# Kernel optimization log

Hardware: AMD Instinct MI355X
Metric: run time of the kernel (lower is better)

Reference implementation:

```python
import jax, jax.numpy as jnp
import numpy as np

NEG_SLOPE = 0.2


def gat_conv(x, edge_index, W, att_src, att_dst, bias, concat):
    # PyG GATConv with add_self_loops=True, negative_slope=0.2
    N = x.shape[0]
    H, C = att_src.shape
    h = (x @ W).reshape(N, H, C)                      # [N, H, C]
    loops = jnp.arange(N, dtype=edge_index.dtype)
    src = jnp.concatenate([edge_index[0], loops])     # [E+N]
    dst = jnp.concatenate([edge_index[1], loops])
    a_src = jnp.einsum('nhc,hc->nh', h, att_src)      # [N, H]
    a_dst = jnp.einsum('nhc,hc->nh', h, att_dst)
    e = jax.nn.leaky_relu(a_src[src] + a_dst[dst], NEG_SLOPE)  # [E+N, H]
    # segment softmax over destination neighborhoods
    e_max = jax.ops.segment_max(e, dst, num_segments=N)        # [N, H]
    e_exp = jnp.exp(e - e_max[dst])
    denom = jax.ops.segment_sum(e_exp, dst, num_segments=N)    # [N, H]
    alpha = e_exp / denom[dst]                                  # [E+N, H]
    msg = h[src] * alpha[:, :, None]                            # [E+N, H, C]
    out = jax.ops.segment_sum(msg, dst, num_segments=N)        # [N, H, C]
    if concat:
        out = out.reshape(N, H * C)
    else:
        out = out.mean(axis=1)
    return out + bias


def setup_inputs() -> dict:
    key = jax.random.key(0)
    ks = jax.random.split(key, 12)
    N, E = 100000, 1600000
    IN, HID, HEADS = 8, 32, 4
    x = jax.random.normal(ks[0], (N, IN), dtype=jnp.float32)
    edge_index = jax.random.randint(ks[1], (2, E), 0, N, dtype=jnp.int32)
    s = 0.1
    W1 = jax.random.normal(ks[2], (IN, HEADS * HID), dtype=jnp.float32) * s
    att_src1 = jax.random.normal(ks[3], (HEADS, HID), dtype=jnp.float32) * s
    att_dst1 = jax.random.normal(ks[4], (HEADS, HID), dtype=jnp.float32) * s
    bias1 = jnp.zeros((HEADS * HID,), dtype=jnp.float32)
    W2 = jax.random.normal(ks[5], (HEADS * HID, HEADS * HID), dtype=jnp.float32) * s
    att_src2 = jax.random.normal(ks[6], (HEADS, HID), dtype=jnp.float32) * s
    att_dst2 = jax.random.normal(ks[7], (HEADS, HID), dtype=jnp.float32) * s
    bias2 = jnp.zeros((HID,), dtype=jnp.float32)
    W_lin = jax.random.normal(ks[8], (HID, 1), dtype=jnp.float32) * s
    b_lin = jnp.zeros((1,), dtype=jnp.float32)
    return {"x": x, "edge_index": edge_index,
            "W1": W1, "att_src1": att_src1, "att_dst1": att_dst1, "bias1": bias1,
            "W2": W2, "att_src2": att_src2, "att_dst2": att_dst2, "bias2": bias2,
            "W_lin": W_lin, "b_lin": b_lin}


def reference(x, edge_index, W1, att_src1, att_dst1, bias1,
              W2, att_src2, att_dst2, bias2, W_lin, b_lin):
    h = gat_conv(x, edge_index, W1, att_src1, att_dst1, bias1, concat=True)
    h = jax.nn.relu(h)
    # dropout p=0.2 is a no-op in eval mode
    h = gat_conv(h, edge_index, W2, att_src2, att_dst2, bias2, concat=False)
    h = jax.nn.relu(h)
    out = h @ W_lin + b_lin
    return out.reshape(-1)
```

## Files before the change

kernel.cpp:

```cpp
#include <hip/hip_runtime.h>

#define NEG_SLOPE 0.2f
#define K1 1024
#define S1B 512

typedef __attribute__((ext_vector_type(8))) short bf16x8;
typedef __attribute__((ext_vector_type(4))) float f32x4;

__device__ __forceinline__ unsigned short f2b(float f) {
    unsigned int u = __float_as_uint(f);
    u += 0x7FFFu + ((u >> 16) & 1u);
    return (unsigned short)(u >> 16);
}
__device__ __forceinline__ float blo(unsigned int u) { return __uint_as_float(u << 16); }
__device__ __forceinline__ float bhi(unsigned int u) { return __uint_as_float(u & 0xFFFF0000u); }

__global__ __launch_bounds__(256) void k_hist(
    const int* __restrict__ ei, int E, int EN,
    int* __restrict__ counts_t,
    const float* __restrict__ x, const float* __restrict__ W1,
    const float* __restrict__ as1, const float* __restrict__ ad1,
    float* __restrict__ asrc, float* __restrict__ adst,
    const float* __restrict__ W2, unsigned short* __restrict__ W2p,
    int N, int AB)
{
    int b = blockIdx.x;
    int t = threadIdx.x;
    if (b < S1B) {
        __shared__ int h[K1];
        for (int k = t; k < K1; k += 256) h[k] = 0;
        __syncthreads();
        int chunk = (EN + S1B - 1) / S1B;
        int lo = b * chunk, hi = min(lo + chunk, EN);
        for (int e = lo + t; e < hi; e += 256) {
            int dst = (e < E) ? ei[E + e] : (e - E);
            atomicAdd(&h[dst >> 7], 1);
        }
        __syncthreads();
        for (int k = t; k < K1; k += 256)
            counts_t[(size_t)k * S1B + b] = h[k];
        return;
    }
    if (b < S1B + AB) {
        __shared__ float s_wa[32], s_wd[32];
        if (t < 32) {
            int k = t >> 2, hh = t & 3;
            float sa = 0.f, sd = 0.f;
            for (int cc = 0; cc < 32; cc++) {
                float w = W1[k * 128 + hh * 32 + cc];
                sa = fmaf(w, as1[hh * 32 + cc], sa);
                sd = fmaf(w, ad1[hh * 32 + cc], sd);
            }
            s_wa[t] = sa;
            s_wd[t] = sd;
        }
        __syncthreads();
        int g = (b - S1B) * 256 + t;
        int n = g >> 2;
        if (n >= N) return;
        int hh = g & 3;
        const float* xr = x + (size_t)n * 8;
        float sa = 0.f, sd = 0.f;
        #pragma unroll
        for (int k = 0; k < 8; k++) {
            float xv = xr[k];
            sa = fmaf(xv, s_wa[k * 4 + hh], sa);
            sd = fmaf(xv, s_wd[k * 4 + hh], sd);
        }
        asrc[n * 4 + hh] = sa;
        adst[n * 4 + hh] = sd;
        return;
    }
    int w = t >> 6, lane = t & 63;
    int quad = lane >> 4, lanelo = lane & 15;
    int tile_n = b - S1B - AB;
    size_t base = (((size_t)tile_n * 4 + w) * 64 + lane) * 8;
    #pragma unroll
    for (int j = 0; j < 8; j++) {
        int k = w * 32 + quad * 8 + j;
        int n = tile_n * 16 + lanelo;
        W2p[base + j] = f2b(W2[k * 128 + n]);
    }
}

__global__ __launch_bounds__(S1B) void k_cscan(
    int* __restrict__ counts_t, int* __restrict__ T)
{
    __shared__ int s[S1B];
    int k = blockIdx.x, t = threadIdx.x;
    int v = counts_t[(size_t)k * S1B + t];
    s[t] = v;
    __syncthreads();
    for (int off = 1; off < S1B; off <<= 1) {
        int u = (t >= off) ? s[t - off] : 0;
        __syncthreads();
        s[t] += u;
        __syncthreads();
    }
    counts_t[(size_t)k * S1B + t] = s[t] - v;
    if (t == S1B - 1) T[k] = s[t];
}

__device__ __forceinline__ void tofs_scan(const int* __restrict__ T,
                                          int* sT, int* ps, int t)
{
    int base = t * 4;
    int s0 = T[base], s1 = T[base + 1], s2 = T[base + 2], s3 = T[base + 3];
    int tot = s0 + s1 + s2 + s3;
    ps[t] = tot;
    __syncthreads();
    for (int off = 1; off < 256; off <<= 1) {
        int u = (t >= off) ? ps[t - off] : 0;
        __syncthreads();
        ps[t] += u;
        __syncthreads();
    }
    int excl = ps[t] - tot;
    sT[base]     = excl;
    sT[base + 1] = excl + s0;
    sT[base + 2] = excl + s0 + s1;
    sT[base + 3] = excl + s0 + s1 + s2;
    __syncthreads();
}

__global__ __launch_bounds__(256) void k_place2(
    const int* __restrict__ ei, int E, int EN,
    const int* __restrict__ counts_t, const int* __restrict__ T,
    unsigned int* __restrict__ tmp)
{
    __shared__ int sT[K1];
    __shared__ int ps[256];
    __shared__ int cur[K1];
    int b = blockIdx.x, t = threadIdx.x;
    tofs_scan(T, sT, ps, t);
    for (int k = t; k < K1; k += 256)
        cur[k] = sT[k] + counts_t[(size_t)k * S1B + b];
    __syncthreads();
    int chunk = (EN + S1B - 1) / S1B;
    int lo = b * chunk, hi = min(lo + chunk, EN);
    for (int e = lo + t; e < hi; e += 256) {
        int src, dst;
        if (e < E) { src = ei[e]; dst = ei[E + e]; }
        else       { src = dst = e - E; }
        int pos = atomicAdd(&cur[dst >> 7], 1);
        tmp[pos] = ((unsigned int)src << 7) | (unsigned int)(dst & 127);
    }
}

__global__ __launch_bounds__(256) void k_fine(
    const unsigned int* __restrict__ tmp, const int* __restrict__ T,
    int* __restrict__ esrc, int* __restrict__ rowptr, int N, int EN)
{
    __shared__ int sT[K1];
    __shared__ int ps[256];
    __shared__ int hist[128], scn[128];
    int k = blockIdx.x, t = threadIdx.x;
    tofs_scan(T, sT, ps, t);
    int lo = sT[k];
    int hi = (k == K1 - 1) ? EN : sT[k + 1];
    int nbase = k << 7;
    if (k == K1 - 1 && t == 0) rowptr[N] = EN;
    if (nbase >= N) return;

    if (t < 128) hist[t] = 0;
    __syncthreads();
    for (int i = lo + t; i < hi; i += 256)
        atomicAdd(&hist[tmp[i] & 127], 1);
    __syncthreads();
    int v = (t < 128) ? hist[t] : 0;
    if (t < 128) scn[t] = v;
    __syncthreads();
    for (int off = 1; off < 128; off <<= 1) {
        int u = (t >= off && t < 128) ? scn[t - off] : 0;
        __syncthreads();
        if (t < 128) scn[t] += u;
        __syncthreads();
    }
    if (t < 128) {
        int ofs = scn[t] - v;
        int dst = nbase + t;
        if (dst < N) rowptr[dst] = lo + ofs;
        hist[t] = ofs;
    }
    __syncthreads();
    for (int i = lo + t; i < hi; i += 256) {
        unsigned int e = tmp[i];
        int r = atomicAdd(&hist[e & 127], 1);
        esrc[lo + r] = (int)(e >> 7);
    }
}

__global__ __launch_bounds__(256) void k_l1f2(
    const int* __restrict__ rowptr, const int* __restrict__ esrc,
    const float* __restrict__ x,
    const float* __restrict__ asrc1, const float* __restrict__ adst1,
    const float* __restrict__ W1, const float* __restrict__ bias1,
    const unsigned short* __restrict__ W2p,
    const float* __restrict__ att_src, const float* __restrict__ att_dst,
    unsigned short* __restrict__ h, float* __restrict__ asrc2,
    float* __restrict__ adst2, int N)
{
    __shared__ float s_y[32][36];
    __shared__ float s_d[32][4];
    __shared__ uint4 s_tile[512];
    char* s_a = reinterpret_cast<char*>(s_tile);
    int t = threadIdx.x;
    int mbase = blockIdx.x * 32;

    {
        int nl = t >> 3;
        int node = mbase + nl;
        if (node >= N) node = N - 1;
        int l8 = t & 7;
        int eo = l8 & 3;
        int dh = (l8 >> 2) << 2;
        const float4* a4p = reinterpret_cast<const float4*>(asrc1);
        float4 ad4 = *reinterpret_cast<const float4*>(adst1 + (size_t)node * 4);
        float acc[4][4];
        #pragma unroll
        for (int hh = 0; hh < 4; hh++)
            #pragma unroll
            for (int c = 0; c < 4; c++) acc[hh][c] = 0.f;
        float d4[4] = {0.f, 0.f, 0.f, 0.f};
        int start = rowptr[node], end = rowptr[node + 1];
        int jj = start + eo;
        for (; jj + 4 < end; jj += 8) {
            int s0 = esrc[jj], s1 = esrc[jj + 4];
            float4 a0 = a4p[s0], a1 = a4p[s1];
            float4 x0 = *reinterpret_cast<const float4*>(x + (size_t)s0 * 8 + dh);
            float4 x1 = *reinterpret_cast<const float4*>(x + (size_t)s1 * 8 + dh);
            float w0[4], w1[4];
            float a;
            a = a0.x + ad4.x; a = a > 0.f ? a : NEG_SLOPE * a; w0[0] = __expf(a);
            a = a0.y + ad4.y; a = a > 0.f ? a : NEG_SLOPE * a; w0[1] = __expf(a);
            a = a0.z + ad4.z; a = a > 0.f ? a : NEG_SLOPE * a; w0[2] = __expf(a);
            a = a0.w + ad4.w; a = a > 0.f ? a : NEG_SLOPE * a; w0[3] = __expf(a);
            a = a1.x + ad4.x; a = a > 0.f ? a : NEG_SLOPE * a; w1[0] = __expf(a);
            a = a1.y + ad4.y; a = a > 0.f ? a : NEG_SLOPE * a; w1[1] = __expf(a);
            a = a1.z + ad4.z; a = a > 0.f ? a : NEG_SLOPE * a; w1[2] = __expf(a);
            a = a1.w + ad4.w; a = a > 0.f ? a : NEG_SLOPE * a; w1[3] = __expf(a);
            #pragma unroll
            for (int hh = 0; hh < 4; hh++) {
                acc[hh][0] = fmaf(w0[hh], x0.x, acc[hh][0]);
                acc[hh][1] = fmaf(w0[hh], x0.y, acc[hh][1]);
                acc[hh][2] = fmaf(w0[hh], x0.z, acc[hh][2]);
                acc[hh][3] = fmaf(w0[hh], x0.w, acc[hh][3]);
                acc[hh][0] = fmaf(w1[hh], x1.x, acc[hh][0]);
                acc[hh][1] = fmaf(w1[hh], x1.y, acc[hh][1]);
                acc[hh][2] = fmaf(w1[hh], x1.z, acc[hh][2]);
                acc[hh][3] = fmaf(w1[hh], x1.w, acc[hh][3]);
                d4[hh] += w0[hh] + w1[hh];
            }
        }
        if (jj < end) {
            int s0 = esrc[jj];
            float4 a0 = a4p[s0];
            float4 x0 = *reinterpret_cast<const float4*>(x + (size_t)s0 * 8 + dh);
            float w0[4];
            float a;
            a = a0.x + ad4.x; a = a > 0.f ? a : NEG_SLOPE * a; w0[0] = __expf(a);
            a = a0.y + ad4.y; a = a > 0.f ? a : NEG_SLOPE * a; w0[1] = __expf(a);
            a = a0.z + ad4.z; a = a > 0.f ? a : NEG_SLOPE * a; w0[2] = __expf(a);
            a = a0.w + ad4.w; a = a > 0.f ? a : NEG_SLOPE * a; w0[3] = __expf(a);
            #pragma unroll
            for (int hh = 0; hh < 4; hh++) {
                acc[hh][0] = fmaf(w0[hh], x0.x, acc[hh][0]);
                acc[hh][1] = fmaf(w0[hh], x0.y, acc[hh][1]);
                acc[hh][2] = fmaf(w0[hh], x0.z, acc[hh][2]);
                acc[hh][3] = fmaf(w0[hh], x0.w, acc[hh][3]);
                d4[hh] += w0[hh];
            }
        }
        #pragma unroll
        for (int hh = 0; hh < 4; hh++) {
            #pragma unroll
            for (int c = 0; c < 4; c++) {
                acc[hh][c] += __shfl_xor(acc[hh][c], 1, 64);
                acc[hh][c] += __shfl_xor(acc[hh][c], 2, 64);
            }
            d4[hh] += __shfl_xor(d4[hh], 1, 64);
            d4[hh] += __shfl_xor(d4[hh], 2, 64);
        }
        if (eo == 0) {
            #pragma unroll
            for (int hh = 0; hh < 4; hh++) {
                float4 o = {acc[hh][0], acc[hh][1], acc[hh][2], acc[hh][3]};
                *reinterpret_cast<float4*>(&s_y[nl][hh * 8 + dh]) = o;
            }
            if (dh == 0) {
                float4 od = {d4[0], d4[1], d4[2], d4[3]};
                *reinterpret_cast<float4*>(&s_d[nl][0]) = od;
            }
        }
    }
    __syncthreads();

    {
        int nl = t >> 3;
        int seg = t & 7;
        int head = seg >> 1;
        float inv = 1.f / s_d[nl][head];
        float y8[8];
        #pragma unroll
        for (int k = 0; k < 8; k++) y8[k] = s_y[nl][head * 8 + k];
        int c0 = seg * 16;
        float acc16[16];
        #pragma unroll
        for (int c = 0; c < 16; c++) acc16[c] = 0.f;
        #pragma unroll
        for (int k = 0; k < 8; k++) {
            float yk = y8[k];
            const float4* wr = reinterpret_cast<const float4*>(W1 + k * 128 + c0);
            #pragma unroll
            for (int q = 0; q < 4; q++) {
                float4 wv = wr[q];
                acc16[q * 4 + 0] = fmaf(yk, wv.x, acc16[q * 4 + 0]);
                acc16[q * 4 + 1] = fmaf(yk, wv.y, acc16[q * 4 + 1]);
                acc16[q * 4 + 2] = fmaf(yk, wv.z, acc16[q * 4 + 2]);
                acc16[q * 4 + 3] = fmaf(yk, wv.w, acc16[q * 4 + 3]);
            }
        }
        unsigned int dw[8];
        #pragma unroll
        for (int c = 0; c < 8; c++) {
            float v0 = acc16[2 * c]     * inv + bias1[c0 + 2 * c];
            float v1 = acc16[2 * c + 1] * inv + bias1[c0 + 2 * c + 1];
            v0 = v0 > 0.f ? v0 : 0.f;
            v1 = v1 > 0.f ? v1 : 0.f;
            dw[c] = ((unsigned int)f2b(v1) << 16) | f2b(v0);
        }
        int byte0 = nl * 256 + seg * 32;
        int swz = (nl & 7) << 4;
        *reinterpret_cast<uint4*>(&s_a[byte0 ^ swz]) =
            make_uint4(dw[0], dw[1], dw[2], dw[3]);
        *reinterpret_cast<uint4*>(&s_a[(byte0 + 16) ^ swz]) =
            make_uint4(dw[4], dw[5], dw[6], dw[7]);
    }
    __syncthreads();

    int w = t >> 6;
    int lane = t & 63;
    int quad = lane >> 4, lanelo = lane & 15;
    int wcb = w * 32;

    f32x4 acc[2][2];
    #pragma unroll
    for (int rt = 0; rt < 2; rt++)
        #pragma unroll
        for (int ct = 0; ct < 2; ct++)
            acc[rt][ct] = (f32x4){0.f, 0.f, 0.f, 0.f};

    #pragma unroll
    for (int kc = 0; kc < 4; kc++) {
        bf16x8 a[2], b[2];
        #pragma unroll
        for (int rt = 0; rt < 2; rt++) {
            int nl = rt * 16 + lanelo;
            int byte = nl * 256 + kc * 64 + quad * 16;
            a[rt] = *reinterpret_cast<const bf16x8*>(&s_a[byte ^ ((nl & 7) << 4)]);
        }
        #pragma unroll
        for (int ct = 0; ct < 2; ct++) {
            int tile_n = w * 2 + ct;
            b[ct] = *reinterpret_cast<const bf16x8*>(
                W2p + (((size_t)tile_n * 4 + kc) * 64 + lane) * 8);
        }
        #pragma unroll
        for (int rt = 0; rt < 2; rt++)
            #pragma unroll
            for (int ct = 0; ct < 2; ct++)
                acc[rt][ct] = __builtin_amdgcn_mfma_f32_16x16x32_bf16(
                    a[rt], b[ct], acc[rt][ct], 0, 0, 0);
    }

    float as_[2], ad_[2];
    #pragma unroll
    for (int ct = 0; ct < 2; ct++) {
        int col = wcb + ct * 16 + lanelo;
        as_[ct] = att_src[col];
        ad_[ct] = att_dst[col];
    }
    #pragma unroll
    for (int rt = 0; rt < 2; rt++) {
        #pragma unroll
        for (int reg = 0; reg < 4; reg++) {
            int node = mbase + rt * 16 + quad * 4 + reg;
            bool ok = node < N;
            float v0 = acc[rt][0][reg], v1 = acc[rt][1][reg];
            if (ok) {
                h[(size_t)node * 128 + wcb + lanelo]      = f2b(v0);
                h[(size_t)node * 128 + wcb + 16 + lanelo] = f2b(v1);
            }
            float ps = v0 * as_[0] + v1 * as_[1];
            float pd = v0 * ad_[0] + v1 * ad_[1];
            #pragma unroll
            for (int off = 8; off >= 1; off >>= 1) {
                ps += __shfl_xor(ps, off, 64);
                pd += __shfl_xor(pd, off, 64);
            }
            if (ok && lanelo == 0) {
                asrc2[node * 4 + w] = ps;
                adst2[node * 4 + w] = pd;
            }
        }
    }
}

__device__ __forceinline__ void agg_edge(float w, uint4 u, float acc[8])
{
    acc[0] = fmaf(w, blo(u.x), acc[0]); acc[1] = fmaf(w, bhi(u.x), acc[1]);
    acc[2] = fmaf(w, blo(u.y), acc[2]); acc[3] = fmaf(w, bhi(u.y), acc[3]);
    acc[4] = fmaf(w, blo(u.z), acc[4]); acc[5] = fmaf(w, bhi(u.z), acc[5]);
    acc[6] = fmaf(w, blo(u.w), acc[6]); acc[7] = fmaf(w, bhi(u.w), acc[7]);
}

__device__ __forceinline__ void agg_core16(
    int n, int l4,
    const int* __restrict__ rowptr, const int* __restrict__ esrc,
    const uint4* __restrict__ h ,
    const float* __restrict__ asrc, const float* __restrict__ adst,
    float acc[8], float& d)
{
    int head = l4 >> 2;
    float ad = adst[n * 4 + head];
    #pragma unroll
    for (int k = 0; k < 8; k++) acc[k] = 0.f;
    d = 0.f;
    int j = rowptr[n], end = rowptr[n + 1];

    for (; j + 4 <= end; j += 4) {
        int s0 = esrc[j], s1 = esrc[j + 1], s2 = esrc[j + 2], s3 = esrc[j + 3];
        float A0 = asrc[s0 * 4 + head];
        float A1 = asrc[s1 * 4 + head];
        float A2 = asrc[s2 * 4 + head];
        float A3 = asrc[s3 * 4 + head];
        uint4 u0 = h[(size_t)s0 * 16 + l4];
        uint4 u1 = h[(size_t)s1 * 16 + l4];
        uint4 u2 = h[(size_t)s2 * 16 + l4];
        uint4 u3 = h[(size_t)s3 * 16 + l4];
        A0 += ad; A0 = A0 > 0.f ? A0 : NEG_SLOPE * A0; float w0 = __expf(A0);
        A1 += ad; A1 = A1 > 0.f ? A1 : NEG_SLOPE * A1; float w1 = __expf(A1);
        A2 += ad; A2 = A2 > 0.f ? A2 : NEG_SLOPE * A2; float w2 = __expf(A2);
        A3 += ad; A3 = A3 > 0.f ? A3 : NEG_SLOPE * A3; float w3 = __expf(A3);
        agg_edge(w0, u0, acc); d += w0;
        agg_edge(w1, u1, acc); d += w1;
        agg_edge(w2, u2, acc); d += w2;
        agg_edge(w3, u3, acc); d += w3;
    }
    for (; j < end; j++) {
        int src = esrc[j];
        float a = asrc[src * 4 + head] + ad;
        a = a > 0.f ? a : NEG_SLOPE * a;
        float w = __expf(a);
        uint4 u = h[(size_t)src * 16 + l4];
        agg_edge(w, u, acc); d += w;
    }
}

__global__ __launch_bounds__(256) void k_agg2(
    const int* __restrict__ rowptr, const int* __restrict__ esrc,
    const uint4* __restrict__ h, const float* __restrict__ asrc,
    const float* __restrict__ adst, const float* __restrict__ bias2,
    const float* __restrict__ Wlin, const float* __restrict__ blin,
    float* __restrict__ out, int N)
{
    int gid = blockIdx.x * 256 + threadIdx.x;
    int node = gid >> 4;
    if (node >= N) return;
    int l4 = threadIdx.x & 15;
    float acc[8], d;
    agg_core16(node, l4, rowptr, esrc, h, asrc, adst, acc, d);
    float inv = 1.f / d;
    float v[8];
    #pragma unroll
    for (int k = 0; k < 8; k++) v[k] = acc[k] * inv;
    #pragma unroll
    for (int k = 0; k < 8; k++) {
        v[k] += __shfl_xor(v[k], 4, 64);
        v[k] += __shfl_xor(v[k], 8, 64);
    }
    int cc = (l4 & 3) * 8;
    const float4 b0 = *reinterpret_cast<const float4*>(bias2 + cc);
    const float4 b1 = *reinterpret_cast<const float4*>(bias2 + cc + 4);
    const float4 w0 = *reinterpret_cast<const float4*>(Wlin + cc);
    const float4 w1 = *reinterpret_cast<const float4*>(Wlin + cc + 4);
    float bb[8] = {b0.x, b0.y, b0.z, b0.w, b1.x, b1.y, b1.z, b1.w};
    float ww[8] = {w0.x, w0.y, w0.z, w0.w, w1.x, w1.y, w1.z, w1.w};
    float t = 0.f;
    #pragma unroll
    for (int k = 0; k < 8; k++) {
        float m = 0.25f * v[k] + bb[k];
        float y = m > 0.f ? m : 0.f;
        t = fmaf(y, ww[k], t);
    }
    t += __shfl_xor(t, 1, 64);
    t += __shfl_xor(t, 2, 64);
    if (l4 == 0) out[node] = t + blin[0];
}

extern "C" void kernel_launch(void* const* d_in, const int* in_sizes, int n_in,
                              void* d_out, int out_size, void* d_ws, size_t ws_size,
                              hipStream_t stream)
{
    const float* x   = (const float*)d_in[0];
    const int*   ei  = (const int*)  d_in[1];
    const float* W1  = (const float*)d_in[2];
    const float* as1 = (const float*)d_in[3];
    const float* ad1 = (const float*)d_in[4];
    const float* b1  = (const float*)d_in[5];
    const float* W2  = (const float*)d_in[6];
    const float* as2 = (const float*)d_in[7];
    const float* ad2 = (const float*)d_in[8];
    const float* b2  = (const float*)d_in[9];
    const float* Wl  = (const float*)d_in[10];
    const float* bl  = (const float*)d_in[11];
    float* out = (float*)d_out;

    int N  = in_sizes[0] / 8;
    int E  = in_sizes[1] / 2;
    int EN = E + N;

    float* ws    = (float*)d_ws;
    unsigned short* A = (unsigned short*)ws;
    float* asrc1 = ws + (size_t)N * 64;
    float* adst1 = asrc1 + (size_t)N * 4;
    float* asrc2 = adst1 + (size_t)N * 4;
    float* adst2 = asrc2 + (size_t)N * 4;
    int* rowptr  = (int*)(adst2 + (size_t)N * 4);
    int* esrc    = rowptr + (N + 1);
    int* counts_t = esrc + EN;
    int* T       = counts_t + (size_t)K1 * S1B;
    unsigned short* W2p = (unsigned short*)(T + K1);
    unsigned int* tmp = (unsigned int*)(W2p + 16384);

    int ab = (N + 63) / 64;
    int nb = (N + 15) / 16;

    k_hist<<<S1B + ab + 8, 256, 0, stream>>>(ei, E, EN, counts_t,
                                             x, W1, as1, ad1, asrc1, adst1,
                                             W2, W2p, N, ab);
    k_cscan<<<K1, S1B, 0, stream>>>(counts_t, T);
    k_place2<<<S1B, 256, 0, stream>>>(ei, E, EN, counts_t, T, tmp);
    k_fine<<<K1, 256, 0, stream>>>(tmp, T, esrc, rowptr, N, EN);

    k_l1f2<<<(N + 31) / 32, 256, 0, stream>>>(rowptr, esrc, x, asrc1, adst1,
                                              W1, b1, W2p, as2, ad2,
                                              A, asrc2, adst2, N);
    k_agg2<<<nb, 256, 0, stream>>>(rowptr, esrc, (const uint4*)A,
                                   asrc2, adst2, b2, Wl, bl, out, N);
}
```

Measured before the change: 263.3 us.

## Restructure CSR build as block-local sort plus gather-based fine pass

Replaces the global histogram/scan/scatter pipeline with a per-block local bucket sort that writes edges into the block's own chunk of tmp, records per-bucket offset/count pairs, sums columns into bucket totals, and has each fine-bucket block gather its segments into LDS before the final per-node sort. This removes one kernel launch and the second full pass over edge_index, and turns scattered global writes into block-local ones. In exchange, the fine pass copies variable-length segments serially per thread, and the 3072-entry staging buffer assumes no bucket exceeds that size, which can overflow on skewed graphs.

Result: faster. 255.9 us (-2.8%).

```diff
diff --git a/kernel.cpp b/kernel.cpp
--- a/kernel.cpp
+++ b/kernel.cpp
@@ -15,9 +15,32 @@
 __device__ __forceinline__ float blo(unsigned int u) { return __uint_as_float(u << 16); }
 __device__ __forceinline__ float bhi(unsigned int u) { return __uint_as_float(u & 0xFFFF0000u); }
 
-__global__ __launch_bounds__(256) void k_hist(
+__device__ __forceinline__ void tofs_scan(const int* __restrict__ T,
+                                          int* sT, int* ps, int t)
+{
+    int base = t * 4;
+    int s0 = T[base], s1 = T[base + 1], s2 = T[base + 2], s3 = T[base + 3];
+    int tot = s0 + s1 + s2 + s3;
+    ps[t] = tot;
+    __syncthreads();
+    for (int off = 1; off < 256; off <<= 1) {
+        int u = (t >= off) ? ps[t - off] : 0;
+        __syncthreads();
+        ps[t] += u;
+        __syncthreads();
+    }
+    int excl = ps[t] - tot;
+    sT[base]     = excl;
+    sT[base + 1] = excl + s0;
+    sT[base + 2] = excl + s0 + s1;
+    sT[base + 3] = excl + s0 + s1 + s2;
+    __syncthreads();
+}
+
+__global__ __launch_bounds__(256) void k_lsort(
     const int* __restrict__ ei, int E, int EN,
-    int* __restrict__ counts_t,
+    int2* __restrict__ pairs,
+    unsigned int* __restrict__ tmp,
     const float* __restrict__ x, const float* __restrict__ W1,
     const float* __restrict__ as1, const float* __restrict__ ad1,
     float* __restrict__ asrc, float* __restrict__ adst,
@@ -27,18 +50,49 @@
     int b = blockIdx.x;
     int t = threadIdx.x;
     if (b < S1B) {
-        __shared__ int h[K1];
-        for (int k = t; k < K1; k += 256) h[k] = 0;
+        __shared__ int hist[K1];
+        __shared__ int ofs[K1];
+        __shared__ int cur[K1];
+        __shared__ int ps[256];
+        for (int k = t; k < K1; k += 256) hist[k] = 0;
         __syncthreads();
         int chunk = (EN + S1B - 1) / S1B;
         int lo = b * chunk, hi = min(lo + chunk, EN);
         for (int e = lo + t; e < hi; e += 256) {
             int dst = (e < E) ? ei[E + e] : (e - E);
-            atomicAdd(&h[dst >> 7], 1);
-        }
-        __syncthreads();
-        for (int k = t; k < K1; k += 256)
-            counts_t[(size_t)k * S1B + b] = h[k];
+            atomicAdd(&hist[dst >> 7], 1);
+        }
+        __syncthreads();
+        int base = t * 4;
+        int h0 = hist[base], h1 = hist[base + 1];
+        int h2 = hist[base + 2], h3 = hist[base + 3];
+        int tot = h0 + h1 + h2 + h3;
+        ps[t] = tot;
+        __syncthreads();
+        for (int off = 1; off < 256; off <<= 1) {
+            int u = (t >= off) ? ps[t - off] : 0;
+            __syncthreads();
+            ps[t] += u;
+            __syncthreads();
+        }
+        int ex = ps[t] - tot;
+        ofs[base]     = ex;
+        ofs[base + 1] = ex + h0;
+        ofs[base + 2] = ex + h0 + h1;
+        ofs[base + 3] = ex + h0 + h1 + h2;
+        __syncthreads();
+        for (int k = t; k < K1; k += 256) {
+            pairs[(size_t)b * K1 + k] = make_int2(ofs[k], hist[k]);
+            cur[k] = ofs[k];
+        }
+        __syncthreads();
+        for (int e = lo + t; e < hi; e += 256) {
+            int src, dst;
+            if (e < E) { src = ei[e]; dst = ei[E + e]; }
+            else       { src = dst = e - E; }
+            int pos = lo + atomicAdd(&cur[dst >> 7], 1);
+            tmp[pos] = ((unsigned int)src << 7) | (unsigned int)(dst & 127);
+        }
         return;
     }
     if (b < S1B + AB) {
@@ -83,89 +137,78 @@
     }
 }
 
-__global__ __launch_bounds__(S1B) void k_cscan(
-    int* __restrict__ counts_t, int* __restrict__ T)
-{
-    __shared__ int s[S1B];
-    int k = blockIdx.x, t = threadIdx.x;
-    int v = counts_t[(size_t)k * S1B + t];
-    s[t] = v;
-    __syncthreads();
-    for (int off = 1; off < S1B; off <<= 1) {
-        int u = (t >= off) ? s[t - off] : 0;
-        __syncthreads();
-        s[t] += u;
-        __syncthreads();
-    }
-    counts_t[(size_t)k * S1B + t] = s[t] - v;
-    if (t == S1B - 1) T[k] = s[t];
-}
-
-__device__ __forceinline__ void tofs_scan(const int* __restrict__ T,
-                                          int* sT, int* ps, int t)
-{
-    int base = t * 4;
-    int s0 = T[base], s1 = T[base + 1], s2 = T[base + 2], s3 = T[base + 3];
-    int tot = s0 + s1 + s2 + s3;
-    ps[t] = tot;
-    __syncthreads();
-    for (int off = 1; off < 256; off <<= 1) {
-        int u = (t >= off) ? ps[t - off] : 0;
-        __syncthreads();
-        ps[t] += u;
-        __syncthreads();
-    }
-    int excl = ps[t] - tot;
-    sT[base]     = excl;
-    sT[base + 1] = excl + s0;
-    sT[base + 2] = excl + s0 + s1;
-    sT[base + 3] = excl + s0 + s1 + s2;
-    __syncthreads();
-}
-
-__global__ __launch_bounds__(256) void k_place2(
-    const int* __restrict__ ei, int E, int EN,
-    const int* __restrict__ counts_t, const int* __restrict__ T,
-    unsigned int* __restrict__ tmp)
+__global__ __launch_bounds__(256) void k_colsum(
+    const int2* __restrict__ pairs, int* __restrict__ T)
+{
+    __shared__ int part[256];
+    int j = blockIdx.x, t = threadIdx.x;
+    int kk = t & 15;
+    int bs = t >> 4;
+    int k = j * 16 + kk;
+    int s = 0;
+    for (int b = bs; b < S1B; b += 16)
+        s += pairs[(size_t)b * K1 + k].y;
+    part[t] = s;
+    __syncthreads();
+    for (int off = 128; off >= 16; off >>= 1) {
+        if (t < off) part[t] += part[t + off];
+        __syncthreads();
+    }
+    if (t < 16) T[j * 16 + t] = part[t];
+}
+
+__global__ __launch_bounds__(256) void k_fine2(
+    const int2* __restrict__ pairs, const unsigned int* __restrict__ tmp,
+    const int* __restrict__ T,
+    int* __restrict__ esrc, int* __restrict__ rowptr, int N, int EN)
 {
     __shared__ int sT[K1];
     __shared__ int ps[256];
-    __shared__ int cur[K1];
-    int b = blockIdx.x, t = threadIdx.x;
-    tofs_scan(T, sT, ps, t);
-    for (int k = t; k < K1; k += 256)
-        cur[k] = sT[k] + counts_t[(size_t)k * S1B + b];
-    __syncthreads();
-    int chunk = (EN + S1B - 1) / S1B;
-    int lo = b * chunk, hi = min(lo + chunk, EN);
-    for (int e = lo + t; e < hi; e += 256) {
-        int src, dst;
-        if (e < E) { src = ei[e]; dst = ei[E + e]; }
-        else       { src = dst = e - E; }
-        int pos = atomicAdd(&cur[dst >> 7], 1);
-        tmp[pos] = ((unsigned int)src << 7) | (unsigned int)(dst & 127);
-    }
-}
-
-__global__ __launch_bounds__(256) void k_fine(
-    const unsigned int* __restrict__ tmp, const int* __restrict__ T,
-    int* __restrict__ esrc, int* __restrict__ rowptr, int N, int EN)
-{
-    __shared__ int sT[K1];
-    __shared__ int ps[256];
+    __shared__ int rofs[S1B], rcnt[S1B], sofs[S1B];
+    __shared__ unsigned int stg[3072];
     __shared__ int hist[128], scn[128];
     int k = blockIdx.x, t = threadIdx.x;
     tofs_scan(T, sT, ps, t);
     int lo = sT[k];
-    int hi = (k == K1 - 1) ? EN : sT[k + 1];
     int nbase = k << 7;
     if (k == K1 - 1 && t == 0) rowptr[N] = EN;
     if (nbase >= N) return;
-
+    int chunk = (EN + S1B - 1) / S1B;
+
+    #pragma unroll
+    for (int i = 0; i < 2; i++) {
+        int b = t + i * 256;
+        int2 pr = pairs[(size_t)b * K1 + k];
+        rofs[b] = pr.x;
+        rcnt[b] = pr.y;
+    }
+    __syncthreads();
+    int c0 = rcnt[2 * t], c1 = rcnt[2 * t + 1];
+    int tot = c0 + c1;
+    ps[t] = tot;
+    __syncthreads();
+    for (int off = 1; off < 256; off <<= 1) {
+        int u = (t >= off) ? ps[t - off] : 0;
+        __syncthreads();
+        ps[t] += u;
+        __syncthreads();
+    }
+    int ex = ps[t] - tot;
+    sofs[2 * t] = ex;
+    sofs[2 * t + 1] = ex + c0;
+    __syncthreads();
+    int total = sofs[S1B - 1] + rcnt[S1B - 1];
+    #pragma unroll
+    for (int i = 0; i < 2; i++) {
+        int b = t + i * 256;
+        int n0 = rcnt[b], o = sofs[b];
+        const unsigned int* srcp = tmp + (size_t)b * chunk + rofs[b];
+        for (int q = 0; q < n0; q++) stg[o + q] = srcp[q];
+    }
     if (t < 128) hist[t] = 0;
     __syncthreads();
-    for (int i = lo + t; i < hi; i += 256)
-        atomicAdd(&hist[tmp[i] & 127], 1);
+    for (int i = t; i < total; i += 256)
+        atomicAdd(&hist[stg[i] & 127], 1);
     __syncthreads();
     int v = (t < 128) ? hist[t] : 0;
     if (t < 128) scn[t] = v;
@@ -177,14 +220,14 @@
         __syncthreads();
     }
     if (t < 128) {
-        int ofs = scn[t] - v;
+        int o = scn[t] - v;
         int dst = nbase + t;
-        if (dst < N) rowptr[dst] = lo + ofs;
-        hist[t] = ofs;
-    }
-    __syncthreads();
-    for (int i = lo + t; i < hi; i += 256) {
-        unsigned int e = tmp[i];
+        if (dst < N) rowptr[dst] = lo + o;
+        hist[t] = o;
+    }
+    __syncthreads();
+    for (int i = t; i < total; i += 256) {
+        unsigned int e = stg[i];
         int r = atomicAdd(&hist[e & 127], 1);
         esrc[lo + r] = (int)(e >> 7);
     }
@@ -528,20 +571,21 @@
     float* adst2 = asrc2 + (size_t)N * 4;
     int* rowptr  = (int*)(adst2 + (size_t)N * 4);
     int* esrc    = rowptr + (N + 1);
-    int* counts_t = esrc + EN;
-    int* T       = counts_t + (size_t)K1 * S1B;
+    int* T       = esrc + EN;
     unsigned short* W2p = (unsigned short*)(T + K1);
-    unsigned int* tmp = (unsigned int*)(W2p + 16384);
+    uintptr_t pp = (uintptr_t)(W2p + 16384);
+    pp = (pp + 7) & ~(uintptr_t)7;
+    int2* pairs  = (int2*)pp;
+    unsigned int* tmp = (unsigned int*)(pairs + (size_t)S1B * K1);
 
     int ab = (N + 63) / 64;
     int nb = (N + 15) / 16;
 
-    k_hist<<<S1B + ab + 8, 256, 0, stream>>>(ei, E, EN, counts_t,
-                                             x, W1, as1, ad1, asrc1, adst1,
-                                             W2, W2p, N, ab);
-    k_cscan<<<K1, S1B, 0, stream>>>(counts_t, T);
-    k_place2<<<S1B, 256, 0, stream>>>(ei, E, EN, counts_t, T, tmp);
-    k_fine<<<K1, 256, 0, stream>>>(tmp, T, esrc, rowptr, N, EN);
+    k_lsort<<<S1B + ab + 8, 256, 0, stream>>>(ei, E, EN, pairs, tmp,
+                                              x, W1, as1, ad1, asrc1, adst1,
+                                              W2, W2p, N, ab);
+    k_colsum<<<K1 / 16, 256, 0, stream>>>(pairs, T);
+    k_fine2<<<K1, 256, 0, stream>>>(pairs, tmp, T, esrc, rowptr, N, EN);
 
     k_l1f2<<<(N + 31) / 32, 256, 0, stream>>>(rowptr, esrc, x, asrc1, adst1,
                                               W1, b1, W2p, as2, ad2,
```
